# Kernel optimization log

Measured on AMD Instinct MI355X. Metric: run time of the kernel, lower is better.

## Reference

```python
import jax, jax.numpy as jnp
import numpy as np

E = 2048
H = 16
D = E // H  # head_dim = 128
S_SLOTS = 8
EPS = 1e-5


def _linear_params(key, fan_in, fan_out):
    kw, kb = jax.random.split(key)
    lim = 1.0 / np.sqrt(fan_in)
    W = jax.random.uniform(kw, (fan_out, fan_in), jnp.float32, -lim, lim)
    b = jax.random.uniform(kb, (fan_out,), jnp.float32, -lim, lim)
    return W, b


def setup_inputs() -> dict:
    key = jax.random.key(0)
    ks = jax.random.split(key, 10)
    x = jax.random.normal(ks[0], (2, 2048, E), jnp.float32)
    thought_slots = jax.random.normal(ks[1], (S_SLOTS, E), jnp.float32)
    Wq, bq = _linear_params(ks[2], E, E)
    Wk, bk = _linear_params(ks[3], E, E)
    Wv, bv = _linear_params(ks[4], E, E)
    Wtq, btq = _linear_params(ks[5], E, E)
    Wtk, btk = _linear_params(ks[6], E, E)
    Wtv, btv = _linear_params(ks[7], E, E)
    Wo, bo = _linear_params(ks[8], E, E)
    gamma = jnp.ones((E,), jnp.float32)
    beta = jnp.zeros((E,), jnp.float32)
    return dict(x=x, thought_slots=thought_slots, Wq=Wq, bq=bq, Wk=Wk, bk=bk,
                Wv=Wv, bv=bv, Wtq=Wtq, btq=btq, Wtk=Wtk, btk=btk,
                Wtv=Wtv, btv=btv, Wo=Wo, bo=bo, gamma=gamma, beta=beta)


def _heads(t, B):
    # [B, S, E] -> [B, H, S, D]
    return t.reshape(B, -1, H, D).transpose(0, 2, 1, 3)


def reference(x, thought_slots, Wq, bq, Wk, bk, Wv, bv,
              Wtq, btq, Wtk, btk, Wtv, btv, Wo, bo, gamma, beta):
    B, S, _ = x.shape
    scale = 1.0 / np.sqrt(D)

    # regular self-attention stream
    q = _heads(x @ Wq.T + bq, B)
    k = _heads(x @ Wk.T + bk, B)
    v = _heads(x @ Wv.T + bv, B)
    attn = jax.nn.softmax(jnp.einsum('bhqd,bhkd->bhqk', q, k) * scale, axis=-1)
    regular_out = jnp.einsum('bhqk,bhkd->bhqd', attn, v)

    # thought cross-attention stream (keys/values from learned slots)
    slots = jnp.broadcast_to(thought_slots, (B, S_SLOTS, thought_slots.shape[-1]))
    t_q = _heads(x @ Wtq.T + btq, B)
    t_k = _heads(slots @ Wtk.T + btk, B)
    t_v = _heads(slots @ Wtv.T + btv, B)
    t_attn = jax.nn.softmax(jnp.einsum('bhqd,bhkd->bhqk', t_q, t_k) * scale, axis=-1)
    thought_out = jnp.einsum('bhqk,bhkd->bhqd', t_attn, t_v)

    # merge heads, combine, layernorm, output projection
    combined = (regular_out + thought_out).transpose(0, 2, 1, 3).reshape(B, S, E)
    mu = jnp.mean(combined, axis=-1, keepdims=True)
    var = jnp.var(combined, axis=-1, keepdims=True)
    normed = (combined - mu) * jax.lax.rsqrt(var + EPS) * gamma + beta
    return normed @ Wo.T + bo
```

## Files before the change

kernel.cpp:

```cpp
#include <hip/hip_runtime.h>
#include <hip/hip_bf16.h>
#include <stdint.h>

typedef __bf16 bf16;
typedef __bf16 bf16x8 __attribute__((ext_vector_type(8)));
typedef __bf16 bf16x4 __attribute__((ext_vector_type(4)));
typedef float f32x4 __attribute__((ext_vector_type(4)));
typedef float f32x16 __attribute__((ext_vector_type(16)));
typedef uint32_t u32x2 __attribute__((ext_vector_type(2)));
typedef uint32_t u32x4 __attribute__((ext_vector_type(4)));

#define E_DIM 2048
#define HEADS 16
#define HD 128
#define SEQ 2048
#define BATCH 2
#define NTOK 4096
#define NSLOT 8

#define QSCALE (0.08838834764831845f * 1.4426950408889634f)

#define WAITV(N) asm volatile("s_waitcnt vmcnt(" #N ")" ::: "memory")

__device__ __forceinline__ void gload_lds16(const void* g, void* lds) {
  __builtin_amdgcn_global_load_lds(
      (const __attribute__((address_space(1))) uint32_t*)g,
      (__attribute__((address_space(3))) uint32_t*)lds, 16, 0, 0);
}

__global__ __launch_bounds__(256) void cvt_f32_bf16_kernel(
    const float* __restrict__ src, bf16* __restrict__ dst, int n8)
{
  for (int i = blockIdx.x * 256 + threadIdx.x; i < n8; i += gridDim.x * 256) {
    const f32x4 a = *(const f32x4*)(src + i * 8);
    const f32x4 b = *(const f32x4*)(src + i * 8 + 4);
    bf16x8 o;
#pragma unroll
    for (int j = 0; j < 4; j++) { o[j] = (bf16)a[j]; o[4 + j] = (bf16)b[j]; }
    *(bf16x8*)(dst + i * 8) = o;
  }
}

struct ProjArgs {
  const bf16* W[4];
  const float* bias[4];
  void* out[4];
  int mode[4];
  float scale[4];
};

__global__ __launch_bounds__(512, 2) void gemm256_kernel(
    const bf16* __restrict__ A, ProjArgs pa, int nbm, int nbn)
{
  __shared__ char LdsA[2 * 2 * 16384];
  __shared__ char LdsB[2 * 2 * 16384];

  const int nwg = gridDim.x;
  const int qch = nwg >> 3;
  const int wg = (blockIdx.x & 7) * qch + (blockIdx.x >> 3);
  const int bm = wg % nbm;
  const int rest = wg / nbm;
  const int bn = rest % nbn;
  const int z = rest / nbn;

  const bf16* __restrict__ W = pa.W[z];
  const float* __restrict__ bias = pa.bias[z];
  void* __restrict__ out = pa.out[z];
  const int mode = pa.mode[z];
  const float scale = pa.scale[z];

  const int tid = threadIdx.x;
  const int lane = tid & 63;
  const int w = tid >> 6;
  const int wr = w >> 2;
  const int wc = w & 3;
  const int g = lane >> 4, c = lane & 15;

  const int rw = tid >> 2;
  const int sc = (((tid & 3) ^ ((rw >> 1) & 3))) * 8;
  const bf16* Asrc = A + (size_t)(bm * 256 + rw) * 2048 + sc;
  const bf16* Bsrc = W + (size_t)(bn * 256 + rw) * 2048 + sc;

  auto stage = [&](int T, int s) {
    const int q4 = ((T & 1) * 2 + s) * 16384;
    const int k0 = T * 64 + s * 32;
#pragma unroll
    for (int j = 0; j < 2; j++) {
      gload_lds16(Asrc + (size_t)(j * 128) * 2048 + k0, LdsA + q4 + j * 8192 + tid * 16);
      gload_lds16(Bsrc + (size_t)(j * 128) * 2048 + k0, LdsB + q4 + j * 8192 + tid * 16);
    }
  };

  f32x4 acc[8][4] = {};
  const int fsw = (c >> 1) & 3;

  stage(0, 0); stage(0, 1); stage(1, 0);
  WAITV(8);
  __builtin_amdgcn_s_barrier();

  const int NT = 2048 / 64;
  for (int t = 0; t < NT; t++) {
    const int d = t & 1;
#pragma unroll
    for (int ph = 0; ph < 2; ph++) {
      if (ph == 0) { if (t + 1 < NT) stage(t + 1, 1); }
      else         { if (t + 2 < NT) stage(t + 2, 0); }

      const char* Aq = LdsA + (d * 2 + ph) * 16384;
      const char* Bq = LdsB + (d * 2 + ph) * 16384;
      bf16x8 af[8], bfr[4];
#pragma unroll
      for (int n = 0; n < 4; n++) {
        const int row = wc * 64 + n * 16 + c;
        bfr[n] = *(const bf16x8*)(Bq + row * 64 + ((g ^ fsw) * 16));
      }
#pragma unroll
      for (int mi = 0; mi < 8; mi++) {
        const int row = wr * 128 + mi * 16 + c;
        af[mi] = *(const bf16x8*)(Aq + row * 64 + ((g ^ fsw) * 16));
      }
      __builtin_amdgcn_s_setprio(1);
#pragma unroll
      for (int mi = 0; mi < 8; mi++)
#pragma unroll
        for (int n = 0; n < 4; n++)
          acc[mi][n] = __builtin_amdgcn_mfma_f32_16x16x32_bf16(af[mi], bfr[n], acc[mi][n], 0, 0, 0);
      __builtin_amdgcn_s_setprio(0);

      if (ph == 0) {
        if (t == NT - 1) { WAITV(0); } else { WAITV(8); }
        __builtin_amdgcn_s_barrier();
      } else {
        if (t < NT - 2)       { WAITV(8); __builtin_amdgcn_s_barrier(); }
        else if (t == NT - 2) { WAITV(4); __builtin_amdgcn_s_barrier(); }
      }
    }
  }

#pragma unroll
  for (int mi = 0; mi < 8; mi++) {
#pragma unroll
    for (int n = 0; n < 4; n++) {
      const int col = bn * 256 + wc * 64 + n * 16 + c;
      const float bv = bias[col];
#pragma unroll
      for (int j = 0; j < 4; j++) {
        const int row = bm * 256 + wr * 128 + mi * 16 + g * 4 + j;
        const float v = (acc[mi][n][j] + bv) * scale;
        if (mode == 0) {
          ((float*)out)[(size_t)row * E_DIM + col] = v;
        } else {
          const int b = row >> 11, s = row & 2047;
          const int h = col >> 7, d2 = col & 127;
          size_t idx;
          if (mode == 1) idx = (((size_t)(b * HEADS + h)) * SEQ + s) * HD + d2;
          else           idx = (((size_t)(b * HEADS + h)) * HD + d2) * SEQ + s;
          ((bf16*)out)[idx] = (bf16)v;
        }
      }
    }
  }
}

__global__ __launch_bounds__(256) void gemm_nt_kernel(
    const bf16* __restrict__ A, ProjArgs pa, int M, int N, int K)
{
  __shared__ bf16 As[2][128 * 32];
  __shared__ bf16 Bs[2][128 * 32];

  const int z = blockIdx.z;
  const bf16* __restrict__ W = pa.W[z];
  const float* __restrict__ bias = pa.bias[z];
  void* __restrict__ out = pa.out[z];
  const int mode = pa.mode[z];
  const float scale = pa.scale[z];

  const int tid = threadIdx.x;
  const int lane = tid & 63;
  const int w = tid >> 6;
  const int wr = w >> 1, wc = w & 1;
  const int g = lane >> 4, c = lane & 15;
  const int bm = blockIdx.x, bn = blockIdx.y;

  f32x4 acc[4][4] = {};

  const int srow = lane >> 2;
  const int scol = (lane & 3) * 8;
  const bf16* Ab = A + (size_t)(bm * 128 + srow) * K + scol;
  const bf16* Wb = W + (size_t)(bn * 128 + srow) * K + scol;

  auto stage = [&](int k0, int buf) {
#pragma unroll
    for (int i = 0; i < 2; ++i) {
      const int chunk = w * 2 + i;
      gload_lds16(Ab + (size_t)(chunk * 16) * K + k0, (char*)(&As[buf][0]) + chunk * 1024);
      gload_lds16(Wb + (size_t)(chunk * 16) * K + k0, (char*)(&Bs[buf][0]) + chunk * 1024);
    }
  };

  stage(0, 0);
  __syncthreads();
  int cur = 0;

  for (int k0 = 0; k0 < K; k0 += 32) {
    if (k0 + 32 < K) stage(k0 + 32, cur ^ 1);
    bf16x8 af[4], bfr[4];
#pragma unroll
    for (int m = 0; m < 4; m++)
      af[m] = *(const bf16x8*)(&As[cur][0] + (wr * 64 + m * 16 + c) * 32 + g * 8);
#pragma unroll
    for (int n = 0; n < 4; n++)
      bfr[n] = *(const bf16x8*)(&Bs[cur][0] + (wc * 64 + n * 16 + c) * 32 + g * 8);
#pragma unroll
    for (int m = 0; m < 4; m++)
#pragma unroll
      for (int n = 0; n < 4; n++)
        acc[m][n] = __builtin_amdgcn_mfma_f32_16x16x32_bf16(af[m], bfr[n], acc[m][n], 0, 0, 0);
    __syncthreads();
    cur ^= 1;
  }

#pragma unroll
  for (int m = 0; m < 4; m++) {
#pragma unroll
    for (int n = 0; n < 4; n++) {
      const int col = bn * 128 + wc * 64 + n * 16 + c;
      const float bv = bias[col];
#pragma unroll
      for (int j = 0; j < 4; j++) {
        const int row = bm * 128 + wr * 64 + m * 16 + g * 4 + j;
        const float v = (acc[m][n][j] + bv) * scale;
        if (mode == 0) {
          ((float*)out)[(size_t)row * N + col] = v;
        } else {
          const int b = row >> 11, s = row & 2047;
          const int h = col >> 7, d = col & 127;
          size_t idx;
          if (mode == 1) idx = (((size_t)(b * HEADS + h)) * SEQ + s) * HD + d;
          else           idx = (((size_t)(b * HEADS + h)) * HD + d) * SEQ + s;
          ((bf16*)out)[idx] = (bf16)v;
        }
      }
    }
  }
}

__global__ __launch_bounds__(256) void slots_proj_kernel(
    const float* __restrict__ slots,
    const float* __restrict__ Wk, const float* __restrict__ bk,
    const float* __restrict__ Wv, const float* __restrict__ bv,
    float* __restrict__ tk, float* __restrict__ tv)
{
  const int col = blockIdx.x * 256 + threadIdx.x;
  const int slot = blockIdx.y;
  const int mat = blockIdx.z;
  const float* W = mat ? Wv : Wk;
  const float* bias = mat ? bv : bk;
  float* out = mat ? tv : tk;
  const float* xr = slots + (size_t)slot * E_DIM;
  const float* wr = W + (size_t)col * E_DIM;
  float acc = 0.f;
  for (int k = 0; k < E_DIM; k += 4) {
    const f32x4 a = *(const f32x4*)(xr + k);
    const f32x4 b4 = *(const f32x4*)(wr + k);
#pragma unroll
    for (int i = 0; i < 4; i++) acc += a[i] * b4[i];
  }
  out[(size_t)slot * E_DIM + col] = acc + bias[col];
}

__global__ __launch_bounds__(512) void flash_attn_kernel(
    const bf16* __restrict__ Qg, const bf16* __restrict__ Kg,
    const bf16* __restrict__ Vtg, bf16* __restrict__ Og)
{
  __shared__ char Ks[2][64 * 256];
  __shared__ char Vs[2][128 * 128];

  const int orig = blockIdx.x;
  const int logical = (orig & 7) * 32 + (orig >> 3);
  const int qt = logical & 7;
  const int bh = logical >> 3;

  const int tid = threadIdx.x;
  const int lane = tid & 63;
  const int w = tid >> 6;
  const int q = lane & 31;
  const int hi = lane >> 5;
  const int b = bh >> 4, h = bh & 15;
  const int q0 = qt * 256 + w * 32;

  const bf16* Qb = Qg + ((size_t)bh * SEQ + q0) * HD;
  const bf16* Kb = Kg + (size_t)bh * SEQ * HD;
  const bf16* Vb = Vtg + (size_t)bh * HD * SEQ;

  auto stage = [&](int kv0, int buf) {
#pragma unroll
    for (int i = 0; i < 2; i++) {
      const int p = (tid + i * 512) * 16;
      { const int r = p >> 8; const int s16 = (p >> 4) & 15;
        gload_lds16(Kb + (size_t)(kv0 + r) * HD + (s16 ^ (r & 15)) * 8, &Ks[buf][0] + p); }
      { const int r = p >> 7; const int s8 = (p >> 4) & 7;
        gload_lds16(Vb + (size_t)r * SEQ + kv0 + (s8 ^ (r & 7)) * 8, &Vs[buf][0] + p); }
    }
  };

  bf16x8 qf[8];
#pragma unroll
  for (int kc = 0; kc < 8; kc++)
    qf[kc] = *(const bf16x8*)(Qb + (size_t)q * HD + kc * 16 + hi * 8);

  stage(0, 0);
  __syncthreads();
  int cur = 0;

  f32x16 o[4] = {};
  float mrun = -1e30f, lsum = 0.f;

  for (int kv0 = 0; kv0 < SEQ; kv0 += 64) {
    if (kv0 + 64 < SEQ) stage(kv0 + 64, cur ^ 1);

    f32x16 st[2] = {};
    __builtin_amdgcn_s_setprio(1);
#pragma unroll
    for (int kc = 0; kc < 8; kc++) {
#pragma unroll
      for (int blk = 0; blk < 2; blk++) {
        const int rt = blk * 32 + q;
        const int sl = (2 * kc + hi) ^ (rt & 15);
        const bf16x8 kf = *(const bf16x8*)(&Ks[cur][0] + rt * 256 + sl * 16);
        st[blk] = __builtin_amdgcn_mfma_f32_32x32x16_bf16(kf, qf[kc], st[blk], 0, 0, 0);
      }
    }
    __builtin_amdgcn_s_setprio(0);

    float t[16];
#pragma unroll
    for (int i = 0; i < 16; i++) t[i] = fmaxf(st[0][i], st[1][i]);
#pragma unroll
    for (int s2 = 8; s2 > 0; s2 >>= 1)
#pragma unroll
      for (int i = 0; i < 8; i++) if (i < s2) t[i] = fmaxf(t[i], t[i + s2]);
    float lm = t[0];
    lm = fmaxf(lm, __shfl_xor(lm, 32));

    float fsc = 1.0f;
    if (__any(lm > mrun + 8.0f)) {
      const float mn = fmaxf(mrun, lm);
      fsc = exp2f(mrun - mn);
      mrun = mn;
#pragma unroll
      for (int db = 0; db < 4; db++)
#pragma unroll
        for (int i = 0; i < 16; i++) o[db][i] *= fsc;
    }

    float ps0 = 0.f, ps1 = 0.f, ps2 = 0.f, ps3 = 0.f;
#pragma unroll
    for (int blk = 0; blk < 2; blk++)
#pragma unroll
      for (int i = 0; i < 16; i += 4) {
        const float p0 = exp2f(st[blk][i]     - mrun);
        const float p1 = exp2f(st[blk][i + 1] - mrun);
        const float p2 = exp2f(st[blk][i + 2] - mrun);
        const float p3 = exp2f(st[blk][i + 3] - mrun);
        st[blk][i] = p0; st[blk][i + 1] = p1; st[blk][i + 2] = p2; st[blk][i + 3] = p3;
        ps0 += p0; ps1 += p1; ps2 += p2; ps3 += p3;
      }
    lsum = lsum * fsc + ((ps0 + ps1) + (ps2 + ps3));

    bf16x8 pb[2][2];
#pragma unroll
    for (int blk = 0; blk < 2; blk++)
#pragma unroll
      for (int c2 = 0; c2 < 2; c2++) {
        bf16x4 Lv, Hv;
#pragma unroll
        for (int i = 0; i < 4; i++) {
          Lv[i] = (bf16)st[blk][8 * c2 + i];
          Hv[i] = (bf16)st[blk][8 * c2 + 4 + i];
        }
        const u32x2 Lu = __builtin_bit_cast(u32x2, Lv);
        const u32x2 Hu = __builtin_bit_cast(u32x2, Hv);
        const uint32_t s0 = hi ? Lu.x : Hu.x;
        const uint32_t s1 = hi ? Lu.y : Hu.y;
        const uint32_t x0 = (uint32_t)__shfl_xor((int)s0, 32);
        const uint32_t x1 = (uint32_t)__shfl_xor((int)s1, 32);
        u32x4 bv;
        bv.x = hi ? x0 : Lu.x;
        bv.y = hi ? x1 : Lu.y;
        bv.z = hi ? Hu.x : x0;
        bv.w = hi ? Hu.y : x1;
        pb[blk][c2] = __builtin_bit_cast(bf16x8, bv);
      }

    __builtin_amdgcn_s_setprio(1);
#pragma unroll
    for (int db = 0; db < 4; db++) {
      const int rt = db * 32 + q;
#pragma unroll
      for (int blk = 0; blk < 2; blk++)
#pragma unroll
        for (int c2 = 0; c2 < 2; c2++) {
          const int sl = (blk * 4 + c2 * 2 + hi) ^ (rt & 7);
          const bf16x8 vf = *(const bf16x8*)(&Vs[cur][0] + rt * 128 + sl * 16);
          o[db] = __builtin_amdgcn_mfma_f32_32x32x16_bf16(vf, pb[blk][c2], o[db], 0, 0, 0);
        }
    }
    __builtin_amdgcn_s_setprio(0);

    __syncthreads();
    cur ^= 1;
  }

  const float lt = lsum + __shfl_xor(lsum, 32);
  const float linv = 1.0f / lt;
  bf16* Orow = Og + ((size_t)b * SEQ + q0 + q) * E_DIM + h * HD;
#pragma unroll
  for (int db = 0; db < 4; db++)
#pragma unroll
    for (int g4 = 0; g4 < 4; g4++) {
      bf16x4 ov;
#pragma unroll
      for (int i = 0; i < 4; i++) ov[i] = (bf16)(o[db][g4 * 4 + i] * linv);
      *(bf16x4*)(Orow + db * 32 + g4 * 8 + hi * 4) = ov;
    }
}

__global__ __launch_bounds__(256) void thought_ln_kernel(
    const bf16* __restrict__ TQ, const float* __restrict__ TK,
    const float* __restrict__ TV, const bf16* __restrict__ ATT,
    const float* __restrict__ gamma, const float* __restrict__ beta,
    bf16* __restrict__ Y)
{
  __shared__ float wsum[4], wsq[4];
  const int tid = threadIdx.x;
  const int lane = tid & 63;
  const int w = tid >> 6;
  const int tok = blockIdx.x;
  const int b = tok >> 11, s = tok & 2047;
  const int e0 = tid * 8;
  const int h = e0 >> 7;
  const int d0 = e0 & 127;

  const bf16x8 av = *(const bf16x8*)(ATT + (size_t)tok * E_DIM + e0);
  float v[8];
#pragma unroll
  for (int i = 0; i < 8; i++) v[i] = (float)av[i];

  const bf16x8 qv8 = *(const bf16x8*)(TQ + (((size_t)(b * HEADS + h)) * SEQ + s) * HD + d0);
  float qv[8];
#pragma unroll
  for (int i = 0; i < 8; i++) qv[i] = (float)qv8[i];

  float dts[NSLOT];
#pragma unroll
  for (int sl = 0; sl < NSLOT; sl++) {
    const float* tkr = TK + (size_t)sl * E_DIM + e0;
    const f32x4 k0 = *(const f32x4*)(tkr);
    const f32x4 k1 = *(const f32x4*)(tkr + 4);
    float dp = 0.f;
#pragma unroll
    for (int i = 0; i < 4; i++) dp += qv[i] * k0[i] + qv[4 + i] * k1[i];
    dp += __shfl_xor(dp, 1);
    dp += __shfl_xor(dp, 2);
    dp += __shfl_xor(dp, 4);
    dp += __shfl_xor(dp, 8);
    dts[sl] = dp;
  }
  float mx = dts[0];
#pragma unroll
  for (int sl = 1; sl < NSLOT; sl++) mx = fmaxf(mx, dts[sl]);
  float p[NSLOT], den = 0.f;
#pragma unroll
  for (int sl = 0; sl < NSLOT; sl++) { p[sl] = exp2f(dts[sl] - mx); den += p[sl]; }
  const float dinv = 1.0f / den;
#pragma unroll
  for (int sl = 0; sl < NSLOT; sl++) {
    const float pn = p[sl] * dinv;
    const float* tvr = TV + (size_t)sl * E_DIM + e0;
    const f32x4 v0 = *(const f32x4*)(tvr);
    const f32x4 v1 = *(const f32x4*)(tvr + 4);
#pragma unroll
    for (int i = 0; i < 4; i++) { v[i] += pn * v0[i]; v[4 + i] += pn * v1[i]; }
  }

  float sm = 0.f, sq = 0.f;
#pragma unroll
  for (int i = 0; i < 8; i++) { sm += v[i]; sq += v[i] * v[i]; }
#pragma unroll
  for (int d = 1; d < 64; d <<= 1) { sm += __shfl_xor(sm, d); sq += __shfl_xor(sq, d); }
  if (lane == 0) { wsum[w] = sm; wsq[w] = sq; }
  __syncthreads();
  const float ts = wsum[0] + wsum[1] + wsum[2] + wsum[3];
  const float tq2 = wsq[0] + wsq[1] + wsq[2] + wsq[3];
  const float mean = ts * (1.f / E_DIM);
  const float var = tq2 * (1.f / E_DIM) - mean * mean;
  const float rstd = rsqrtf(var + 1e-5f);
  const f32x4 g0 = *(const f32x4*)(gamma + e0);
  const f32x4 g1 = *(const f32x4*)(gamma + e0 + 4);
  const f32x4 b0 = *(const f32x4*)(beta + e0);
  const f32x4 b1 = *(const f32x4*)(beta + e0 + 4);
  bf16x8 outv;
#pragma unroll
  for (int i = 0; i < 4; i++) {
    outv[i]     = (bf16)((v[i]     - mean) * rstd * g0[i] + b0[i]);
    outv[4 + i] = (bf16)((v[4 + i] - mean) * rstd * g1[i] + b1[i]);
  }
  *(bf16x8*)(Y + (size_t)tok * E_DIM + e0) = outv;
}

extern "C" void kernel_launch(void* const* d_in, const int* in_sizes, int n_in,
                              void* d_out, int out_size, void* d_ws, size_t ws_size,
                              hipStream_t stream) {
  (void)in_sizes; (void)n_in; (void)out_size; (void)ws_size;
  const float* x     = (const float*)d_in[0];
  const float* slots = (const float*)d_in[1];
  const float* Wq  = (const float*)d_in[2];   const float* bq  = (const float*)d_in[3];
  const float* Wk  = (const float*)d_in[4];   const float* bk  = (const float*)d_in[5];
  const float* Wv  = (const float*)d_in[6];   const float* bv  = (const float*)d_in[7];
  const float* Wtq = (const float*)d_in[8];   const float* btq = (const float*)d_in[9];
  const float* Wtk = (const float*)d_in[10];  const float* btk = (const float*)d_in[11];
  const float* Wtv = (const float*)d_in[12];  const float* btv = (const float*)d_in[13];
  const float* Wo  = (const float*)d_in[14];  const float* bo  = (const float*)d_in[15];
  const float* gamma = (const float*)d_in[16];
  const float* beta  = (const float*)d_in[17];

  uint8_t* ws = (uint8_t*)d_ws;
  const size_t BUF  = (size_t)NTOK * E_DIM * sizeof(bf16);
  const size_t WBUF = (size_t)E_DIM * E_DIM * sizeof(bf16);
  bf16* xb   = (bf16*)(ws + 0 * BUF);
  bf16* qb   = (bf16*)(ws + 1 * BUF);
  bf16* kb   = (bf16*)(ws + 2 * BUF);
  bf16* vtb  = (bf16*)(ws + 3 * BUF);
  bf16* tqb  = (bf16*)(ws + 4 * BUF);
  bf16* attb = (bf16*)(ws + 5 * BUF);
  bf16* nrmb = qb;
  uint8_t* wp = ws + 6 * BUF;
  bf16* Wqb  = (bf16*)(wp + 0 * WBUF);
  bf16* Wkb  = (bf16*)(wp + 1 * WBUF);
  bf16* Wvb  = (bf16*)(wp + 2 * WBUF);
  bf16* Wtqb = (bf16*)(wp + 3 * WBUF);
  bf16* Wob  = (bf16*)(wp + 4 * WBUF);
  float* tkb = (float*)(wp + 5 * WBUF);
  float* tvb = (float*)(wp + 5 * WBUF + 128 * 1024);

  const int WN8 = E_DIM * E_DIM / 8;
  const int XN8 = NTOK * E_DIM / 8;
  cvt_f32_bf16_kernel<<<dim3(2048), 256, 0, stream>>>(x, xb, XN8);
  cvt_f32_bf16_kernel<<<dim3(1024), 256, 0, stream>>>(Wq, Wqb, WN8);
  cvt_f32_bf16_kernel<<<dim3(1024), 256, 0, stream>>>(Wk, Wkb, WN8);
  cvt_f32_bf16_kernel<<<dim3(1024), 256, 0, stream>>>(Wv, Wvb, WN8);
  cvt_f32_bf16_kernel<<<dim3(1024), 256, 0, stream>>>(Wtq, Wtqb, WN8);
  cvt_f32_bf16_kernel<<<dim3(1024), 256, 0, stream>>>(Wo, Wob, WN8);

  ProjArgs pa;
  pa.W[0] = Wqb;  pa.bias[0] = bq;  pa.out[0] = qb;  pa.mode[0] = 1; pa.scale[0] = QSCALE;
  pa.W[1] = Wkb;  pa.bias[1] = bk;  pa.out[1] = kb;  pa.mode[1] = 1; pa.scale[1] = 1.0f;
  pa.W[2] = Wvb;  pa.bias[2] = bv;  pa.out[2] = vtb; pa.mode[2] = 2; pa.scale[2] = 1.0f;
  pa.W[3] = Wtqb; pa.bias[3] = btq; pa.out[3] = tqb; pa.mode[3] = 1; pa.scale[3] = QSCALE;
  gemm256_kernel<<<dim3(16 * 8 * 4), 512, 0, stream>>>(xb, pa, 16, 8);

  slots_proj_kernel<<<dim3(E_DIM / 256, NSLOT, 2), 256, 0, stream>>>(
      slots, Wtk, btk, Wtv, btv, tkb, tvb);

  flash_attn_kernel<<<dim3((SEQ / 256) * BATCH * HEADS), 512, 0, stream>>>(
      qb, kb, vtb, attb);
  thought_ln_kernel<<<dim3(NTOK), 256, 0, stream>>>(
      tqb, tkb, tvb, attb, gamma, beta, nrmb);

  ProjArgs po;
  po.W[0] = Wob; po.bias[0] = bo; po.out[0] = d_out; po.mode[0] = 0; po.scale[0] = 1.0f;
  po.W[1] = po.W[2] = po.W[3] = Wob;
  po.bias[1] = po.bias[2] = po.bias[3] = bo;
  po.out[1] = po.out[2] = po.out[3] = d_out;
  po.mode[1] = po.mode[2] = po.mode[3] = 0;
  po.scale[1] = po.scale[2] = po.scale[3] = 1.0f;
  gemm_nt_kernel<<<dim3(NTOK / 128, E_DIM / 128, 1), 256, 0, stream>>>(
      nrmb, po, NTOK, E_DIM, E_DIM);
}
```

Baseline: 482.4 us.

## Restructure GEMM mainloop into four sub-phases with full-K-tile LDS staging

Changes the 256x256 GEMM's LDS layout from two 32-wide K halves per stage to one 64-wide row per tile with an 8-slot XOR swizzle. The main loop is split into four quarter-phases, each loading two A row-fragments and issuing one quarter of the global-to-LDS prefetch, so that memory traffic is spread more evenly across the MFMA work. B fragments are now loaded once per tile and held in registers, which cuts LDS reads but raises register pressure. There are now more barriers per tile, and the wait counts have been retuned for the new prefetch order.

Measured after the change: 466.1 us. 3.4% less time.

```diff
diff --git a/kernel.cpp b/kernel.cpp
--- a/kernel.cpp
+++ b/kernel.cpp
@@ -52,8 +52,8 @@
 __global__ __launch_bounds__(512, 2) void gemm256_kernel(
     const bf16* __restrict__ A, ProjArgs pa, int nbm, int nbn)
 {
-  __shared__ char LdsA[2 * 2 * 16384];
-  __shared__ char LdsB[2 * 2 * 16384];
+  __shared__ char As_[2 * 32768];
+  __shared__ char Bs_[2 * 32768];
 
   const int nwg = gridDim.x;
   const int qch = nwg >> 3;
@@ -76,64 +76,83 @@
   const int wc = w & 3;
   const int g = lane >> 4, c = lane & 15;
 
-  const int rw = tid >> 2;
-  const int sc = (((tid & 3) ^ ((rw >> 1) & 3))) * 8;
-  const bf16* Asrc = A + (size_t)(bm * 256 + rw) * 2048 + sc;
-  const bf16* Bsrc = W + (size_t)(bn * 256 + rw) * 2048 + sc;
-
-  auto stage = [&](int T, int s) {
-    const int q4 = ((T & 1) * 2 + s) * 16384;
-    const int k0 = T * 64 + s * 32;
+  const int srow = tid >> 3;
+  const int sslot = tid & 7;
+  const int scol = (sslot ^ (srow & 7)) * 8;
+  const bf16* Abase = A + (size_t)(bm * 256) * 2048;
+  const bf16* Bbase = W + (size_t)(bn * 256) * 2048;
+
+  auto stageU = [&](const bf16* gbase, char* lds, int T, int u) {
+    char* dst = lds + (T & 1) * 32768 + u * 16384;
+    const int k0 = T * 64;
 #pragma unroll
     for (int j = 0; j < 2; j++) {
-      gload_lds16(Asrc + (size_t)(j * 128) * 2048 + k0, LdsA + q4 + j * 8192 + tid * 16);
-      gload_lds16(Bsrc + (size_t)(j * 128) * 2048 + k0, LdsB + q4 + j * 8192 + tid * 16);
+      const int r = u * 128 + srow + j * 64;
+      gload_lds16(gbase + (size_t)r * 2048 + k0 + scol,
+                  dst + (size_t)(srow + j * 64) * 128 + sslot * 16);
     }
   };
 
   f32x4 acc[8][4] = {};
-  const int fsw = (c >> 1) & 3;
-
-  stage(0, 0); stage(0, 1); stage(1, 0);
-  WAITV(8);
+  bf16x8 bfr[4][2];
+
+  stageU(Bbase, Bs_, 0, 0); stageU(Bbase, Bs_, 0, 1);
+  stageU(Abase, As_, 0, 0); stageU(Abase, As_, 0, 1);
+  stageU(Bbase, Bs_, 1, 0); stageU(Bbase, Bs_, 1, 1);
+  stageU(Abase, As_, 1, 0);
+  WAITV(6);
   __builtin_amdgcn_s_barrier();
 
   const int NT = 2048 / 64;
   for (int t = 0; t < NT; t++) {
     const int d = t & 1;
-#pragma unroll
-    for (int ph = 0; ph < 2; ph++) {
-      if (ph == 0) { if (t + 1 < NT) stage(t + 1, 1); }
-      else         { if (t + 2 < NT) stage(t + 2, 0); }
-
-      const char* Aq = LdsA + (d * 2 + ph) * 16384;
-      const char* Bq = LdsB + (d * 2 + ph) * 16384;
-      bf16x8 af[8], bfr[4];
-#pragma unroll
-      for (int n = 0; n < 4; n++) {
-        const int row = wc * 64 + n * 16 + c;
-        bfr[n] = *(const bf16x8*)(Bq + row * 64 + ((g ^ fsw) * 16));
-      }
-#pragma unroll
-      for (int mi = 0; mi < 8; mi++) {
-        const int row = wr * 128 + mi * 16 + c;
-        af[mi] = *(const bf16x8*)(Aq + row * 64 + ((g ^ fsw) * 16));
-      }
+    const char* Aq = As_ + d * 32768;
+    const char* Bq = Bs_ + d * 32768;
+#pragma unroll
+    for (int q = 0; q < 4; q++) {
+      bf16x8 af[2][2];
+      if (q == 0) {
+#pragma unroll
+        for (int n = 0; n < 4; n++)
+#pragma unroll
+          for (int kk = 0; kk < 2; kk++) {
+            const int row = wc * 64 + n * 16 + c;
+            bfr[n][kk] = *(const bf16x8*)(Bq + (size_t)row * 128 +
+                                          (((kk * 4 + g) ^ (c & 7)) * 16));
+          }
+      }
+#pragma unroll
+      for (int mi2 = 0; mi2 < 2; mi2++)
+#pragma unroll
+        for (int kk = 0; kk < 2; kk++) {
+          const int row = wr * 128 + (q * 2 + mi2) * 16 + c;
+          af[mi2][kk] = *(const bf16x8*)(Aq + (size_t)row * 128 +
+                                         (((kk * 4 + g) ^ (c & 7)) * 16));
+        }
+
+      __builtin_amdgcn_s_barrier();
+
+      if (q == 0)      { if (t + 1 < NT) stageU(Abase, As_, t + 1, 1); }
+      else if (q == 1) { if (t + 2 < NT) stageU(Bbase, Bs_, t + 2, 0); }
+      else if (q == 2) { if (t + 2 < NT) stageU(Bbase, Bs_, t + 2, 1); }
+      else             { if (t + 2 < NT) stageU(Abase, As_, t + 2, 0); }
+
       __builtin_amdgcn_s_setprio(1);
 #pragma unroll
-      for (int mi = 0; mi < 8; mi++)
+      for (int mi2 = 0; mi2 < 2; mi2++)
 #pragma unroll
         for (int n = 0; n < 4; n++)
-          acc[mi][n] = __builtin_amdgcn_mfma_f32_16x16x32_bf16(af[mi], bfr[n], acc[mi][n], 0, 0, 0);
+#pragma unroll
+          for (int kk = 0; kk < 2; kk++)
+            acc[q * 2 + mi2][n] = __builtin_amdgcn_mfma_f32_16x16x32_bf16(
+                af[mi2][kk], bfr[n][kk], acc[q * 2 + mi2][n], 0, 0, 0);
       __builtin_amdgcn_s_setprio(0);
 
-      if (ph == 0) {
-        if (t == NT - 1) { WAITV(0); } else { WAITV(8); }
-        __builtin_amdgcn_s_barrier();
-      } else {
-        if (t < NT - 2)       { WAITV(8); __builtin_amdgcn_s_barrier(); }
-        else if (t == NT - 2) { WAITV(4); __builtin_amdgcn_s_barrier(); }
-      }
+      if (q == 3) {
+        if (t < NT - 2)       { WAITV(6); }
+        else if (t == NT - 2) { WAITV(0); }
+      }
+      __builtin_amdgcn_s_barrier();
     }
   }
 
```
